# Performance work log

Hardware: AMD Instinct MI355X
Metric: run time of the kernel (lower is better)

Reference implementation:

```python
import jax, jax.numpy as jnp
import numpy as np

N_NODES = 50000
N_EDGES = 800000
D_FEAT = 64


def setup_inputs() -> dict:
    key = jax.random.key(0)
    k1, k2, k3, k4 = jax.random.split(key, 4)
    row_idx = jnp.sort(jax.random.randint(k1, (N_EDGES,), 0, N_NODES, dtype=jnp.int32))
    col_idx = jax.random.randint(k2, (N_EDGES,), 0, N_NODES, dtype=jnp.int32)
    vals = jax.random.uniform(k3, (N_EDGES,), dtype=jnp.float32)
    embeds = jax.random.normal(k4, (N_NODES, D_FEAT), dtype=jnp.float32)
    return {"row_idx": row_idx, "col_idx": col_idx, "vals": vals, "embeds": embeds}


def reference(row_idx, col_idx, vals, embeds):
    # SpMM: out[r] = sum_{e: row[e]==r} vals[e] * embeds[col[e]]
    gathered = vals[:, None] * embeds[col_idx]          # [E, D]
    out = jax.ops.segment_sum(gathered, row_idx, num_segments=N_NODES)  # [N, D]
    return out
```

## Files before the change

kernel.cpp:

```cpp
#include <hip/hip_runtime.h>
#include <hip/hip_fp16.h>


constexpr int N_NODES = 50000;
constexpr int N_EDGES = 800000;
constexpr int D_FEAT  = 64;

using half4 = __attribute__((ext_vector_type(4))) _Float16;
using half8 = __attribute__((ext_vector_type(8))) _Float16;
using fvec4 = __attribute__((ext_vector_type(4))) float;

constexpr size_t WS_ROWPTR_OFF = 0;
constexpr size_t WS_TBL_OFF    = 1u << 20;

constexpr int ROWPTR_BLOCKS  = (N_EDGES + 255) / 256;
constexpr int CONVERT_BLOCKS = (N_NODES * 16 + 255) / 256;

__global__ __launch_bounds__(256) void prep_kernel(
    const int*   __restrict__ row_idx,
    const float* __restrict__ embeds,
    int*         __restrict__ row_ptr,
    _Float16*    __restrict__ tbl)
{
    if (blockIdx.x < ROWPTR_BLOCKS) {
        const int e = blockIdx.x * 256 + threadIdx.x;
        if (e >= N_EDGES) return;
        const int r     = row_idx[e];
        const int rprev = (e == 0) ? -1 : row_idx[e - 1];
        for (int q = rprev + 1; q <= r; ++q) row_ptr[q] = e;
        if (e == N_EDGES - 1) {
            for (int q = r + 1; q <= N_NODES; ++q) row_ptr[q] = N_EDGES;
        }
    } else {
        const int t = (blockIdx.x - ROWPTR_BLOCKS) * 256 + threadIdx.x;
        if (t >= N_NODES * 16) return;
        const fvec4 v = __builtin_nontemporal_load(((const fvec4*)embeds) + t);
        half4 hv;
        hv[0] = (_Float16)v.x; hv[1] = (_Float16)v.y;
        hv[2] = (_Float16)v.z; hv[3] = (_Float16)v.w;
        ((half4*)tbl)[t] = hv;
    }
}

__global__ __launch_bounds__(256) void gcn_spmm_kernel(
    const int*      __restrict__ row_ptr,
    const int*      __restrict__ col_idx,
    const float*    __restrict__ vals,
    const _Float16* __restrict__ tbl,
    float*          __restrict__ out)
{
    const int row = blockIdx.x * 4 + (threadIdx.x >> 6);
    if (row >= N_NODES) return;

    const int lane = threadIdx.x & 63;
    const int g    = lane >> 3;
    const int h    = lane & 7;

    const int es = row_ptr[row];
    const int ee = row_ptr[row + 1];

    const half8* __restrict__ tbl8 = (const half8*)tbl;

    float acc[8] = {0.f, 0.f, 0.f, 0.f, 0.f, 0.f, 0.f, 0.f};

    for (int base = es; base < ee; base += 16) {
        const int e0 = base + g;
        const int e1 = base + 8 + g;
        const int c0i = (e0 < ee) ? e0 : (ee - 1);
        const int c1i = (e1 < ee) ? e1 : (ee - 1);
        const int   c0 = __builtin_nontemporal_load(col_idx + c0i);
        const int   c1 = __builtin_nontemporal_load(col_idx + c1i);
        const float v0 = (e0 < ee) ? __builtin_nontemporal_load(vals + c0i) : 0.f;
        const float v1 = (e1 < ee) ? __builtin_nontemporal_load(vals + c1i) : 0.f;
        const half8 g0 = tbl8[c0 * 8 + h];
        const half8 g1 = tbl8[c1 * 8 + h];
#pragma unroll
        for (int i = 0; i < 8; ++i) {
            acc[i] += v0 * (float)g0[i];
            acc[i] += v1 * (float)g1[i];
        }
    }

#pragma unroll
    for (int mask = 8; mask <= 32; mask <<= 1) {
#pragma unroll
        for (int i = 0; i < 8; ++i) acc[i] += __shfl_xor(acc[i], mask);
    }

    if (g == 0) {
        fvec4* o4 = (fvec4*)(out + row * D_FEAT + h * 8);
        fvec4 lo, hi;
        lo.x = acc[0]; lo.y = acc[1]; lo.z = acc[2]; lo.w = acc[3];
        hi.x = acc[4]; hi.y = acc[5]; hi.z = acc[6]; hi.w = acc[7];
        __builtin_nontemporal_store(lo, o4);
        __builtin_nontemporal_store(hi, o4 + 1);
    }
}

extern "C" void kernel_launch(void* const* d_in, const int* in_sizes, int n_in,
                              void* d_out, int out_size, void* d_ws, size_t ws_size,
                              hipStream_t stream) {
    const int*   row_idx = (const int*)  d_in[0];
    const int*   col_idx = (const int*)  d_in[1];
    const float* vals    = (const float*)d_in[2];
    const float* embeds  = (const float*)d_in[3];
    float*       out     = (float*)      d_out;

    char* ws = (char*)d_ws;
    int*      row_ptr = (int*)     (ws + WS_ROWPTR_OFF);
    _Float16* tbl     = (_Float16*)(ws + WS_TBL_OFF);

    prep_kernel<<<ROWPTR_BLOCKS + CONVERT_BLOCKS, 256, 0, stream>>>(
        row_idx, embeds, row_ptr, tbl);

    gcn_spmm_kernel<<<(N_NODES + 3) / 4, 256, 0, stream>>>(
        row_ptr, col_idx, vals, tbl, out);
}
```

Baseline: 99.93 us.

## Map one feature per lane with wave-uniform edge indices via readfirstlane

The SpMM kernel now assigns one output feature to each of the 64 lanes instead of splitting edges across 8 lane groups that each hold 8 features. Edge indices and column ids are made wave-uniform with readfirstlane, so they can become scalar loads, and the loop is unrolled by 4 edges. This removes the cross-lane shuffle reduction at the end, and every lane now writes its own output element. In exchange, each gather is a 2-byte-per-lane access with fewer bytes in flight per lane, and edges are processed serially in steps of 4 rather than 16 at a time.

Result: slower. 109.8 us (+9.9%).

```diff
diff --git a/kernel.cpp b/kernel.cpp
--- a/kernel.cpp
+++ b/kernel.cpp
@@ -7,7 +7,6 @@
 constexpr int D_FEAT  = 64;
 
 using half4 = __attribute__((ext_vector_type(4))) _Float16;
-using half8 = __attribute__((ext_vector_type(8))) _Float16;
 using fvec4 = __attribute__((ext_vector_type(4))) float;
 
 constexpr size_t WS_ROWPTR_OFF = 0;
@@ -51,50 +50,40 @@
 {
     const int row = blockIdx.x * 4 + (threadIdx.x >> 6);
     if (row >= N_NODES) return;
+    const int lane = threadIdx.x & 63;
 
-    const int lane = threadIdx.x & 63;
-    const int g    = lane >> 3;
-    const int h    = lane & 7;
+    const int es = __builtin_amdgcn_readfirstlane(row_ptr[row]);
+    const int ee = __builtin_amdgcn_readfirstlane(row_ptr[row + 1]);
 
-    const int es = row_ptr[row];
-    const int ee = row_ptr[row + 1];
+    float acc = 0.f;
 
-    const half8* __restrict__ tbl8 = (const half8*)tbl;
+    for (int e = es; e < ee; e += 4) {
+        const int i1 = (e + 1 < ee) ? e + 1 : ee - 1;
+        const int i2 = (e + 2 < ee) ? e + 2 : ee - 1;
+        const int i3 = (e + 3 < ee) ? e + 3 : ee - 1;
 
-    float acc[8] = {0.f, 0.f, 0.f, 0.f, 0.f, 0.f, 0.f, 0.f};
+        const int c0 = __builtin_amdgcn_readfirstlane(col_idx[e]);
+        const int c1 = __builtin_amdgcn_readfirstlane(col_idx[i1]);
+        const int c2 = __builtin_amdgcn_readfirstlane(col_idx[i2]);
+        const int c3 = __builtin_amdgcn_readfirstlane(col_idx[i3]);
 
-    for (int base = es; base < ee; base += 16) {
-        const int e0 = base + g;
-        const int e1 = base + 8 + g;
-        const int c0i = (e0 < ee) ? e0 : (ee - 1);
-        const int c1i = (e1 < ee) ? e1 : (ee - 1);
-        const int   c0 = __builtin_nontemporal_load(col_idx + c0i);
-        const int   c1 = __builtin_nontemporal_load(col_idx + c1i);
-        const float v0 = (e0 < ee) ? __builtin_nontemporal_load(vals + c0i) : 0.f;
-        const float v1 = (e1 < ee) ? __builtin_nontemporal_load(vals + c1i) : 0.f;
-        const half8 g0 = tbl8[c0 * 8 + h];
-        const half8 g1 = tbl8[c1 * 8 + h];
-#pragma unroll
-        for (int i = 0; i < 8; ++i) {
-            acc[i] += v0 * (float)g0[i];
-            acc[i] += v1 * (float)g1[i];
-        }
+        const float v0 = vals[e];
+        const float v1 = (e + 1 < ee) ? vals[i1] : 0.f;
+        const float v2 = (e + 2 < ee) ? vals[i2] : 0.f;
+        const float v3 = (e + 3 < ee) ? vals[i3] : 0.f;
+
+        const float g0 = (float)tbl[c0 * 64 + lane];
+        const float g1 = (float)tbl[c1 * 64 + lane];
+        const float g2 = (float)tbl[c2 * 64 + lane];
+        const float g3 = (float)tbl[c3 * 64 + lane];
+
+        acc += v0 * g0;
+        acc += v1 * g1;
+        acc += v2 * g2;
+        acc += v3 * g3;
     }
 
-#pragma unroll
-    for (int mask = 8; mask <= 32; mask <<= 1) {
-#pragma unroll
-        for (int i = 0; i < 8; ++i) acc[i] += __shfl_xor(acc[i], mask);
-    }
-
-    if (g == 0) {
-        fvec4* o4 = (fvec4*)(out + row * D_FEAT + h * 8);
-        fvec4 lo, hi;
-        lo.x = acc[0]; lo.y = acc[1]; lo.z = acc[2]; lo.w = acc[3];
-        hi.x = acc[4]; hi.y = acc[5]; hi.z = acc[6]; hi.w = acc[7];
-        __builtin_nontemporal_store(lo, o4);
-        __builtin_nontemporal_store(hi, o4 + 1);
-    }
+    __builtin_nontemporal_store(acc, out + row * D_FEAT + lane);
 }
 
 extern "C" void kernel_launch(void* const* d_in, const int* in_sizes, int n_in,
```
